# Kernel tuning notes

Hardware: AMD Instinct MI355X
Metric: run time of the kernel (lower is better)

Reference implementation:

```python
import jax, jax.numpy as jnp
import numpy as np

B, T, INPUT_DIM, EMBED_DIM = 64, 512, 512, 256


def _lstm_dir(x, mask, k, r, b):
    """Masked unidirectional LSTM (Keras semantics: masked steps carry prev h/c).
    x: [B,T,D], mask: [B,T] bool, k: [D,4U], r: [U,4U], b: [4U]. Returns [B,T,U]."""
    Bx = x.shape[0]
    U = r.shape[0]
    # Precompute input projection once for all timesteps (gate order: i,f,g,o)
    xz = jnp.einsum('btd,dk->btk', x, k) + b          # [B,T,4U]
    xz_t = jnp.swapaxes(xz, 0, 1)                     # [T,B,4U]
    mask_t = jnp.swapaxes(mask, 0, 1)                 # [T,B]
    h0 = jnp.zeros((Bx, U), x.dtype)
    c0 = jnp.zeros((Bx, U), x.dtype)

    def step(carry, inp):
        h, c = carry
        z_x, m = inp
        z = z_x + h @ r                               # [B,4U]
        i, f, g, o = jnp.split(z, 4, axis=-1)
        i = jax.nn.sigmoid(i)
        f = jax.nn.sigmoid(f)
        g = jnp.tanh(g)
        o = jax.nn.sigmoid(o)
        c_new = f * c + i * g
        h_new = o * jnp.tanh(c_new)
        m = m[:, None]
        h2 = jnp.where(m, h_new, h)                   # carry state through masked steps
        c2 = jnp.where(m, c_new, c)
        return (h2, c2), h2

    _, hs = jax.lax.scan(step, (h0, c0), (xz_t, mask_t))
    return jnp.swapaxes(hs, 0, 1)                     # [B,T,U]


def _bilstm_sum(x, mask, kf, rf, bf, kb, rb, bb):
    fwd = _lstm_dir(x, mask, kf, rf, bf)
    # Keras Bidirectional: reverse input and mask, run, reverse output back
    bwd = _lstm_dir(x[:, ::-1], mask[:, ::-1], kb, rb, bb)[:, ::-1]
    return fwd + bwd                                  # merge_mode='sum'


def _lstm_params(key, d_in, units):
    k1, k2, k3 = jax.random.split(key, 3)
    kernel = jax.random.normal(k1, (d_in, 4 * units), jnp.float32) / np.sqrt(d_in)
    rec = jax.random.normal(k2, (units, 4 * units), jnp.float32) / np.sqrt(units)
    bias = jnp.concatenate([
        jnp.zeros((units,), jnp.float32),
        jnp.ones((units,), jnp.float32),              # unit_forget_bias
        jnp.zeros((2 * units,), jnp.float32),
    ])
    return kernel, rec, bias


def setup_inputs() -> dict:
    key = jax.random.key(0)
    ks = jax.random.split(key, 6)
    sequences = jax.random.normal(ks[0], (B, T, INPUT_DIM), jnp.float32)
    sizes = jax.random.randint(ks[1], (B,), 0, T, jnp.int32)
    enc_kf, enc_rf, enc_bf = _lstm_params(ks[2], INPUT_DIM, EMBED_DIM)
    enc_kb, enc_rb, enc_bb = _lstm_params(ks[3], INPUT_DIM, EMBED_DIM)
    dec_kf, dec_rf, dec_bf = _lstm_params(ks[4], EMBED_DIM, INPUT_DIM)
    dec_kb, dec_rb, dec_bb = _lstm_params(ks[5], EMBED_DIM, INPUT_DIM)
    return {
        'sequences': sequences, 'sizes': sizes,
        'enc_kf': enc_kf, 'enc_rf': enc_rf, 'enc_bf': enc_bf,
        'enc_kb': enc_kb, 'enc_rb': enc_rb, 'enc_bb': enc_bb,
        'dec_kf': dec_kf, 'dec_rf': dec_rf, 'dec_bf': dec_bf,
        'dec_kb': dec_kb, 'dec_rb': dec_rb, 'dec_bb': dec_bb,
    }


def reference(sequences, sizes,
              enc_kf, enc_rf, enc_bf, enc_kb, enc_rb, enc_bb,
              dec_kf, dec_rf, dec_bf, dec_kb, dec_rb, dec_bb):
    mask = jnp.arange(sequences.shape[1])[None, :] < sizes[:, None]   # [B,T]
    x = _bilstm_sum(sequences, mask, enc_kf, enc_rf, enc_bf, enc_kb, enc_rb, enc_bb)
    x = _bilstm_sum(x, mask, dec_kf, dec_rf, dec_bf, dec_kb, dec_rb, dec_bb)
    return x
```

## Files before the change

### kernel.cpp

```cpp
#include <hip/hip_runtime.h>
#include <stdint.h>

using short8 = __attribute__((ext_vector_type(8))) short;
using f32x4  = __attribute__((ext_vector_type(4))) float;

#define DEV static __device__ __forceinline__

DEV unsigned short f2bf(float f){
  unsigned u = __builtin_bit_cast(unsigned, f);
  u = (u + 0x7FFFu + ((u >> 16) & 1u)) >> 16;
  return (unsigned short)u;
}
DEV float sigm(float x){
  float e = __builtin_amdgcn_exp2f(-1.4426950408889634f * x);
  return __builtin_amdgcn_rcpf(1.0f + e);
}
DEV float tanh_(float x){
  float e = __builtin_amdgcn_exp2f(2.885390081777927f * x);
  return 1.0f - 2.0f * __builtin_amdgcn_rcpf(e + 1.0f);
}


__global__ void k_f32_to_bf16(const float* __restrict__ in, unsigned short* __restrict__ out, int n){
  int stride = gridDim.x * blockDim.x * 4;
  for (int i = (blockIdx.x * blockDim.x + threadIdx.x) * 4; i < n; i += stride){
    float4 v = *(const float4*)(in + i);
    ushort4 o4;
    o4.x = f2bf(v.x); o4.y = f2bf(v.y); o4.z = f2bf(v.z); o4.w = f2bf(v.w);
    *(ushort4*)(out + i) = o4;
  }
}

__global__ void k_add_bf16(const float* __restrict__ a, const float* __restrict__ b,
                           unsigned short* __restrict__ out, int n){
  int stride = gridDim.x * blockDim.x * 4;
  for (int i = (blockIdx.x * blockDim.x + threadIdx.x) * 4; i < n; i += stride){
    float4 va = *(const float4*)(a + i);
    float4 vb = *(const float4*)(b + i);
    ushort4 o4;
    o4.x = f2bf(va.x + vb.x); o4.y = f2bf(va.y + vb.y);
    o4.z = f2bf(va.z + vb.z); o4.w = f2bf(va.w + vb.w);
    *(ushort4*)(out + i) = o4;
  }
}

__global__ void k_add_f32(float* __restrict__ o, const float* __restrict__ b, int n){
  int stride = gridDim.x * blockDim.x * 4;
  for (int i = (blockIdx.x * blockDim.x + threadIdx.x) * 4; i < n; i += stride){
    float4 vo = *(const float4*)(o + i);
    float4 vb = *(const float4*)(b + i);
    vo.x += vb.x; vo.y += vb.y; vo.z += vb.z; vo.w += vb.w;
    *(float4*)(o + i) = vo;
  }
}

__global__ void k_pack(const float* __restrict__ k0, const float* __restrict__ r0,
                       const float* __restrict__ k1, const float* __restrict__ r1,
                       unsigned short* __restrict__ out, int E, int KX, int U){
  int n = 2 * E;
  int stride = gridDim.x * blockDim.x;
  for (int i = blockIdx.x * blockDim.x + threadIdx.x; i < n; i += stride){
    int d = i / E, r = i % E;
    const float* Km = d ? k1 : k0;
    const float* Rm = d ? r1 : r0;
    int j    = r & 7;  int q = r >> 3;
    int lane = q & 63; q >>= 6;
    int nt   = q & 3;  q >>= 2;
    int kt   = q % 6;  q /= 6;
    int w    = q & 3;  int wg = q >> 2;
    int k    = (w*6 + kt)*32 + ((lane >> 4) << 3) + j;
    int col  = nt * U + wg*16 + (lane & 15);
    float v  = (k < KX) ? Km[(size_t)k * (4*U) + col]
                        : Rm[(size_t)(k - KX) * (4*U) + col];
    out[i] = f2bf(v);
  }
}

template<int KX, int U, int WGS>
__global__ __launch_bounds__(256, 1)
void lstm_rec(const unsigned short* __restrict__ xab,
              const unsigned short* __restrict__ packedB,
              const float* __restrict__ bias_f,
              const float* __restrict__ bias_b,
              const int*   __restrict__ sizes,
              unsigned short* __restrict__ hbuf,
              unsigned int*  __restrict__ counters,
              float* __restrict__ out_f,
              float* __restrict__ out_b)
{
  constexpr int KTW = 6;
  constexpr int T   = 512;

  const int tid  = threadIdx.x;
  const int w    = tid >> 6;
  const int lane = tid & 63;
  const int dir  = (blockIdx.x >= WGS) ? 1 : 0;
  const int wg   = dir ? (int)blockIdx.x - WGS : (int)blockIdx.x;

  const unsigned short* pB = packedB + (size_t)dir * ((size_t)WGS*4*KTW*4*512)
                                     + (size_t)((wg*4 + w)*KTW)*4*512;
  unsigned short* hb  = hbuf + (size_t)dir * (2*64*U);
  unsigned int*   cnt = counters + dir * 32;
  const float* bias = dir ? bias_b : bias_f;
  float* outp       = dir ? out_b : out_f;

  const bool has_h = ((w*KTW + KTW - 1) * 32) >= KX;

  short8 bfr[KTW][4];
  #pragma unroll
  for (int kt = 0; kt < KTW; ++kt)
    #pragma unroll
    for (int nt = 0; nt < 4; ++nt)
      bfr[kt][nt] = *(const short8*)(pB + ((kt*4 + nt)*512) + lane*8);

  const int u_l = tid & 15;
  const int rb  = (tid >> 4) * 4;
  const int ug  = wg*16 + u_l;
  float bz[4]; int sz[4];
  #pragma unroll
  for (int g = 0; g < 4; ++g) bz[g] = bias[g*U + ug];
  #pragma unroll
  for (int r = 0; r < 4; ++r) sz[r] = sizes[rb + r];
  float c[4]    = {0.f,0.f,0.f,0.f};
  float hreg[4] = {0.f,0.f,0.f,0.f};

  __shared__ float part[4][64][68];

  const int arow  = lane & 15;
  const int kgrp  = (lane >> 4) * 8;
  const int rquad = (lane >> 4) * 4;

  short8 areg[KTW][4];
  {
    const int t0 = dir ? T - 1 : 0;
    #pragma unroll
    for (int kt = 0; kt < KTW; ++kt){
      const int kg = (w*KTW + kt) * 32;
      if (kg < KX){
        #pragma unroll
        for (int mt = 0; mt < 4; ++mt)
          areg[kt][mt] = *(const short8*)(xab + ((size_t)((mt*16 + arow)*T + t0))*KX + (kg + kgrp));
      }
    }
  }

  for (int s = 0; s < T; ++s){
    const int t   = dir ? (T - 1 - s) : s;
    const int par = s & 1;

    f32x4 acc[4][4];
    #pragma unroll
    for (int mt = 0; mt < 4; ++mt)
      #pragma unroll
      for (int nt = 0; nt < 4; ++nt)
        acc[mt][nt] = (f32x4){0.f, 0.f, 0.f, 0.f};

    #pragma unroll
    for (int kt = 0; kt < KTW; ++kt){
      const int kg = (w*KTW + kt) * 32;
      if (kg < KX){
        #pragma unroll
        for (int mt = 0; mt < 4; ++mt)
          #pragma unroll
          for (int nt = 0; nt < 4; ++nt)
            acc[mt][nt] = __builtin_amdgcn_mfma_f32_16x16x32_bf16(areg[kt][mt], bfr[kt][nt], acc[mt][nt], 0, 0, 0);
      }
    }

    if (s > 0){
      if (has_h){
        const unsigned tgt = (unsigned)WGS * (unsigned)s;
        for (;;){
          unsigned v = __hip_atomic_load(cnt, __ATOMIC_RELAXED, __HIP_MEMORY_SCOPE_AGENT);
          if (v >= tgt) break;
          __builtin_amdgcn_s_sleep(1);
        }
        __builtin_amdgcn_sched_barrier(0);
        #pragma unroll
        for (int kt = 0; kt < KTW; ++kt){
          const int kg = (w*KTW + kt) * 32;
          if (kg >= KX){
            #pragma unroll
            for (int mt = 0; mt < 4; ++mt){
              const unsigned long long* hp = (const unsigned long long*)
                  (hb + (size_t)par*64*U + (size_t)(mt*16 + arow)*U + (kg - KX + kgrp));
              ulonglong2 u;
              u.x = __hip_atomic_load(hp,     __ATOMIC_RELAXED, __HIP_MEMORY_SCOPE_AGENT);
              u.y = __hip_atomic_load(hp + 1, __ATOMIC_RELAXED, __HIP_MEMORY_SCOPE_AGENT);
              areg[kt][mt] = __builtin_bit_cast(short8, u);
            }
          }
        }
        #pragma unroll
        for (int kt = 0; kt < KTW; ++kt){
          const int kg = (w*KTW + kt) * 32;
          if (kg >= KX){
            #pragma unroll
            for (int mt = 0; mt < 4; ++mt)
              #pragma unroll
              for (int nt = 0; nt < 4; ++nt)
                acc[mt][nt] = __builtin_amdgcn_mfma_f32_16x16x32_bf16(areg[kt][mt], bfr[kt][nt], acc[mt][nt], 0, 0, 0);
          }
        }
      }
    }

    #pragma unroll
    for (int mt = 0; mt < 4; ++mt)
      #pragma unroll
      for (int nt = 0; nt < 4; ++nt)
        *(f32x4*)&part[w][nt*16 + arow][mt*16 + rquad] = acc[mt][nt];

    __syncthreads();

    f32x4 zg[4];
    #pragma unroll
    for (int g = 0; g < 4; ++g){
      const int cb = g*16 + u_l;
      f32x4 v = *(const f32x4*)&part[0][cb][rb];
      #pragma unroll
      for (int ww = 1; ww < 4; ++ww)
        v += *(const f32x4*)&part[ww][cb][rb];
      zg[g] = v;
    }

    #pragma unroll
    for (int r = 0; r < 4; ++r){
      float ig = sigm (zg[0][r] + bz[0]);
      float fg = sigm (zg[1][r] + bz[1]);
      float gg = tanh_(zg[2][r] + bz[2]);
      float og = sigm (zg[3][r] + bz[3]);
      float cn = fg * c[r] + ig * gg;
      float hn = og * tanh_(cn);
      bool m  = (t < sz[r]);
      c[r] = m ? cn : c[r];
      float h = m ? hn : hreg[r];
      hreg[r] = h;
      __hip_atomic_store(&hb[(size_t)(par ^ 1)*64*U + (size_t)(rb + r)*U + ug],
                         (unsigned short)f2bf(h),
                         __ATOMIC_RELAXED, __HIP_MEMORY_SCOPE_AGENT);
    }

    __syncthreads();

    if (s != T - 1){
      if (tid == 0) atomicAdd(cnt, 1u);
    }

    #pragma unroll
    for (int r = 0; r < 4; ++r)
      outp[((size_t)(rb + r)*T + t)*U + ug] = hreg[r];

    if (s != T - 1){
      const int tn = dir ? t - 1 : t + 1;
      #pragma unroll
      for (int kt = 0; kt < KTW; ++kt){
        const int kg = (w*KTW + kt) * 32;
        if (kg < KX){
          #pragma unroll
          for (int mt = 0; mt < 4; ++mt)
            areg[kt][mt] = *(const short8*)(xab + ((size_t)((mt*16 + arow)*T + tn))*KX + (kg + kgrp));
        }
      }
    }
  }
}


extern "C" void kernel_launch(void* const* d_in, const int* in_sizes, int n_in,
                              void* d_out, int out_size, void* d_ws, size_t ws_size,
                              hipStream_t stream){
  const float* x      = (const float*)d_in[0];
  const int*   sizes  = (const int*)  d_in[1];
  const float* enc_kf = (const float*)d_in[2];
  const float* enc_rf = (const float*)d_in[3];
  const float* enc_bf = (const float*)d_in[4];
  const float* enc_kb = (const float*)d_in[5];
  const float* enc_rb = (const float*)d_in[6];
  const float* enc_bb = (const float*)d_in[7];
  const float* dec_kf = (const float*)d_in[8];
  const float* dec_rf = (const float*)d_in[9];
  const float* dec_bf = (const float*)d_in[10];
  const float* dec_kb = (const float*)d_in[11];
  const float* dec_rb = (const float*)d_in[12];
  const float* dec_bb = (const float*)d_in[13];
  float* out = (float*)d_out;
  char*  ws  = (char*)d_ws;

  const size_t o_xbf   = 0;
  const size_t o_esum  = o_xbf   + 33554432ull;
  const size_t o_pBe   = o_esum  + 16777216ull;
  const size_t o_pBd   = o_pBe   + 3145728ull;
  const size_t o_hfe   = o_pBd   + 6291456ull;
  const size_t o_hbe   = o_hfe   + 33554432ull;
  const size_t o_hbd   = o_hbe   + 33554432ull;
  const size_t o_hbufe = o_hbd   + 67108864ull;
  const size_t o_hbufd = o_hbufe + 131072ull;
  const size_t o_cnte  = o_hbufd + 262144ull;
  const size_t o_cntd  = o_cnte  + 4096ull;
  const size_t total   = o_cntd  + 4096ull;
  if (ws_size < total) return;

  unsigned short* xbf   = (unsigned short*)(ws + o_xbf);
  unsigned short* esum  = (unsigned short*)(ws + o_esum);
  unsigned short* pBe   = (unsigned short*)(ws + o_pBe);
  unsigned short* pBd   = (unsigned short*)(ws + o_pBd);
  float*          hfe   = (float*)(ws + o_hfe);
  float*          hbe   = (float*)(ws + o_hbe);
  float*          hbd   = (float*)(ws + o_hbd);
  unsigned short* hbufe = (unsigned short*)(ws + o_hbufe);
  unsigned short* hbufd = (unsigned short*)(ws + o_hbufd);
  unsigned int*   cnte  = (unsigned int*)(ws + o_cnte);
  unsigned int*   cntd  = (unsigned int*)(ws + o_cntd);

  hipMemsetAsync(ws + o_cnte, 0, 8192ull, stream);

  k_f32_to_bf16<<<2048, 256, 0, stream>>>(x, xbf, 64*512*512);

  k_pack<<<2048, 256, 0, stream>>>(enc_kf, enc_rf, enc_kb, enc_rb, pBe, 786432, 512, 256);
  k_pack<<<2048, 256, 0, stream>>>(dec_kf, dec_rf, dec_kb, dec_rb, pBd, 1572864, 256, 512);

  lstm_rec<512, 256, 16><<<32, 256, 0, stream>>>(xbf, pBe, enc_bf, enc_bb, sizes,
                                                 hbufe, cnte, hfe, hbe);
  k_add_bf16<<<2048, 256, 0, stream>>>(hfe, hbe, esum, 64*512*256);

  lstm_rec<256, 512, 32><<<64, 256, 0, stream>>>(esum, pBd, dec_bf, dec_bb, sizes,
                                                 hbufd, cntd, out, hbd);
  k_add_f32<<<2048, 256, 0, stream>>>(out, hbd, 64*512*512);
}
```

Measured before the change: 5.580 ms.

## Replace global step counter with per-element tagged h exchange between workgroups

New measurement: 10.03 ms. +79.8%, slower.

```diff
diff --git a/kernel.cpp b/kernel.cpp
--- a/kernel.cpp
+++ b/kernel.cpp
@@ -3,6 +3,8 @@
 
 using short8 = __attribute__((ext_vector_type(8))) short;
 using f32x4  = __attribute__((ext_vector_type(4))) float;
+using uint4v = __attribute__((ext_vector_type(4))) unsigned;
+typedef unsigned long long ull;
 
 #define DEV static __device__ __forceinline__
 
@@ -11,6 +13,9 @@
   u = (u + 0x7FFFu + ((u >> 16) & 1u)) >> 16;
   return (unsigned short)u;
 }
+DEV float bf2f(unsigned short v){
+  return __builtin_bit_cast(float, ((unsigned)v) << 16);
+}
 DEV float sigm(float x){
   float e = __builtin_amdgcn_exp2f(-1.4426950408889634f * x);
   return __builtin_amdgcn_rcpf(1.0f + e);
@@ -18,6 +23,32 @@
 DEV float tanh_(float x){
   float e = __builtin_amdgcn_exp2f(2.885390081777927f * x);
   return 1.0f - 2.0f * __builtin_amdgcn_rcpf(e + 1.0f);
+}
+
+DEV void bar_lds(){
+  __builtin_amdgcn_sched_barrier(0);
+  asm volatile("s_waitcnt lgkmcnt(0)" ::: "memory");
+  __builtin_amdgcn_s_barrier();
+  __builtin_amdgcn_sched_barrier(0);
+}
+DEV void bar_plain(){
+  __builtin_amdgcn_sched_barrier(0);
+  __builtin_amdgcn_s_barrier();
+  __builtin_amdgcn_sched_barrier(0);
+}
+
+DEV int frag_ok(const ull d0, const ull d1, const ull d2, const ull d3, ull pat){
+  const ull M = 0xFFFF0000FFFF0000ull;
+  ull v = ((d0 & M) ^ pat) | ((d1 & M) ^ pat) | ((d2 & M) ^ pat) | ((d3 & M) ^ pat);
+  return __all(v == 0);
+}
+DEV short8 unpack_h(const ull d0, const ull d1, const ull d2, const ull d3){
+  uint4v u;
+  u[0] = (unsigned)(d0 & 0xFFFFull) | ((unsigned)(d0 >> 32) << 16);
+  u[1] = (unsigned)(d1 & 0xFFFFull) | ((unsigned)(d1 >> 32) << 16);
+  u[2] = (unsigned)(d2 & 0xFFFFull) | ((unsigned)(d2 >> 32) << 16);
+  u[3] = (unsigned)(d3 & 0xFFFFull) | ((unsigned)(d3 >> 32) << 16);
+  return __builtin_bit_cast(short8, u);
 }
 
 
@@ -31,16 +62,17 @@
   }
 }
 
-__global__ void k_add_bf16(const float* __restrict__ a, const float* __restrict__ b,
-                           unsigned short* __restrict__ out, int n){
-  int stride = gridDim.x * blockDim.x * 4;
-  for (int i = (blockIdx.x * blockDim.x + threadIdx.x) * 4; i < n; i += stride){
-    float4 va = *(const float4*)(a + i);
-    float4 vb = *(const float4*)(b + i);
-    ushort4 o4;
-    o4.x = f2bf(va.x + vb.x); o4.y = f2bf(va.y + vb.y);
-    o4.z = f2bf(va.z + vb.z); o4.w = f2bf(va.w + vb.w);
-    *(ushort4*)(out + i) = o4;
+__global__ void k_add_bb(const unsigned short* __restrict__ a, const unsigned short* __restrict__ b,
+                         unsigned short* __restrict__ out, int n){
+  int stride = gridDim.x * blockDim.x * 8;
+  for (int i = (blockIdx.x * blockDim.x + threadIdx.x) * 8; i < n; i += stride){
+    short8 va = *(const short8*)(a + i);
+    short8 vb = *(const short8*)(b + i);
+    short8 o;
+    #pragma unroll
+    for (int j = 0; j < 8; ++j)
+      o[j] = (short)f2bf(bf2f((unsigned short)va[j]) + bf2f((unsigned short)vb[j]));
+    *(short8*)(out + i) = o;
   }
 }
 
@@ -68,7 +100,7 @@
     int nt   = q & 3;  q >>= 2;
     int kt   = q % 6;  q /= 6;
     int w    = q & 3;  int wg = q >> 2;
-    int k    = (w*6 + kt)*32 + ((lane >> 4) << 3) + j;
+    int k    = (kt*4 + w)*32 + ((lane >> 4) << 3) + j;
     int col  = nt * U + wg*16 + (lane & 15);
     float v  = (k < KX) ? Km[(size_t)k * (4*U) + col]
                         : Rm[(size_t)(k - KX) * (4*U) + col];
@@ -76,19 +108,20 @@
   }
 }
 
-template<int KX, int U, int WGS>
+template<int KX, int U, int WGS, bool OBF>
 __global__ __launch_bounds__(256, 1)
 void lstm_rec(const unsigned short* __restrict__ xab,
               const unsigned short* __restrict__ packedB,
               const float* __restrict__ bias_f,
               const float* __restrict__ bias_b,
               const int*   __restrict__ sizes,
-              unsigned short* __restrict__ hbuf,
-              unsigned int*  __restrict__ counters,
-              float* __restrict__ out_f,
-              float* __restrict__ out_b)
+              unsigned* __restrict__ hbuf2,
+              void* __restrict__ out_f,
+              void* __restrict__ out_b)
 {
   constexpr int KTW = 6;
+  constexpr int XKT = KX / 128;
+  constexpr int NH  = KTW - XKT;
   constexpr int T   = 512;
 
   const int tid  = threadIdx.x;
@@ -99,12 +132,9 @@
 
   const unsigned short* pB = packedB + (size_t)dir * ((size_t)WGS*4*KTW*4*512)
                                      + (size_t)((wg*4 + w)*KTW)*4*512;
-  unsigned short* hb  = hbuf + (size_t)dir * (2*64*U);
-  unsigned int*   cnt = counters + dir * 32;
+  unsigned* hb2     = hbuf2 + (size_t)dir * (2*64*U);
   const float* bias = dir ? bias_b : bias_f;
-  float* outp       = dir ? out_b : out_f;
-
-  const bool has_h = ((w*KTW + KTW - 1) * 32) >= KX;
+  void* outp        = dir ? out_b : out_f;
 
   short8 bfr[KTW][4];
   #pragma unroll
@@ -130,23 +160,40 @@
   const int kgrp  = (lane >> 4) * 8;
   const int rquad = (lane >> 4) * 4;
 
-  short8 areg[KTW][4];
+  short8 xreg[XKT][4];
   {
     const int t0 = dir ? T - 1 : 0;
     #pragma unroll
-    for (int kt = 0; kt < KTW; ++kt){
-      const int kg = (w*KTW + kt) * 32;
-      if (kg < KX){
-        #pragma unroll
-        for (int mt = 0; mt < 4; ++mt)
-          areg[kt][mt] = *(const short8*)(xab + ((size_t)((mt*16 + arow)*T + t0))*KX + (kg + kgrp));
-      }
-    }
-  }
+    for (int kt = 0; kt < XKT; ++kt){
+      const int kg = (kt*4 + w) * 32;
+      #pragma unroll
+      for (int mt = 0; mt < 4; ++mt)
+        xreg[kt][mt] = *(const short8*)(xab + ((size_t)((mt*16 + arow)*T + t0))*KX + (kg + kgrp));
+    }
+  }
+
+  ull raw[NH][4][4];
 
   for (int s = 0; s < T; ++s){
     const int t   = dir ? (T - 1 - s) : s;
     const int par = s & 1;
+    const ull tag = (ull)(unsigned)s;
+    const ull pat = (tag << 16) | (tag << 48);
+    const unsigned* hb2r = hb2 + (size_t)par*64*U;
+
+    if (s > 0){
+      #pragma unroll
+      for (int i = 0; i < NH; ++i){
+        const int hu = ((XKT + i)*4 + w)*32 - KX + kgrp;
+        #pragma unroll
+        for (int mt = 0; mt < 4; ++mt){
+          const ull* hp = (const ull*)(hb2r + (size_t)(mt*16 + arow)*U + hu);
+          #pragma unroll
+          for (int j = 0; j < 4; ++j)
+            raw[i][mt][j] = __hip_atomic_load(hp + j, __ATOMIC_RELAXED, __HIP_MEMORY_SCOPE_AGENT);
+        }
+      }
+    }
 
     f32x4 acc[4][4];
     #pragma unroll
@@ -156,54 +203,55 @@
         acc[mt][nt] = (f32x4){0.f, 0.f, 0.f, 0.f};
 
     #pragma unroll
-    for (int kt = 0; kt < KTW; ++kt){
-      const int kg = (w*KTW + kt) * 32;
-      if (kg < KX){
-        #pragma unroll
-        for (int mt = 0; mt < 4; ++mt)
+    for (int kt = 0; kt < XKT; ++kt)
+      #pragma unroll
+      for (int mt = 0; mt < 4; ++mt)
+        #pragma unroll
+        for (int nt = 0; nt < 4; ++nt)
+          acc[mt][nt] = __builtin_amdgcn_mfma_f32_16x16x32_bf16(xreg[kt][mt], bfr[kt][nt], acc[mt][nt], 0, 0, 0);
+
+    if (s > 0){
+      unsigned bad = (1u << (NH*4)) - 1u;
+      for (;;){
+        unsigned nbad = 0;
+        #pragma unroll
+        for (int i = 0; i < NH; ++i)
           #pragma unroll
-          for (int nt = 0; nt < 4; ++nt)
-            acc[mt][nt] = __builtin_amdgcn_mfma_f32_16x16x32_bf16(areg[kt][mt], bfr[kt][nt], acc[mt][nt], 0, 0, 0);
-      }
-    }
-
-    if (s > 0){
-      if (has_h){
-        const unsigned tgt = (unsigned)WGS * (unsigned)s;
-        for (;;){
-          unsigned v = __hip_atomic_load(cnt, __ATOMIC_RELAXED, __HIP_MEMORY_SCOPE_AGENT);
-          if (v >= tgt) break;
-          __builtin_amdgcn_s_sleep(1);
-        }
-        __builtin_amdgcn_sched_barrier(0);
-        #pragma unroll
-        for (int kt = 0; kt < KTW; ++kt){
-          const int kg = (w*KTW + kt) * 32;
-          if (kg >= KX){
-            #pragma unroll
-            for (int mt = 0; mt < 4; ++mt){
-              const unsigned long long* hp = (const unsigned long long*)
-                  (hb + (size_t)par*64*U + (size_t)(mt*16 + arow)*U + (kg - KX + kgrp));
-              ulonglong2 u;
-              u.x = __hip_atomic_load(hp,     __ATOMIC_RELAXED, __HIP_MEMORY_SCOPE_AGENT);
-              u.y = __hip_atomic_load(hp + 1, __ATOMIC_RELAXED, __HIP_MEMORY_SCOPE_AGENT);
-              areg[kt][mt] = __builtin_bit_cast(short8, u);
+          for (int mt = 0; mt < 4; ++mt){
+            const unsigned f = i*4 + mt;
+            if (bad & (1u << f))
+              if (!frag_ok(raw[i][mt][0], raw[i][mt][1], raw[i][mt][2], raw[i][mt][3], pat))
+                nbad |= 1u << f;
+          }
+        if (!nbad) break;
+        #pragma unroll
+        for (int i = 0; i < NH; ++i){
+          const int hu = ((XKT + i)*4 + w)*32 - KX + kgrp;
+          #pragma unroll
+          for (int mt = 0; mt < 4; ++mt){
+            const unsigned f = i*4 + mt;
+            if (nbad & (1u << f)){
+              const ull* hp = (const ull*)(hb2r + (size_t)(mt*16 + arow)*U + hu);
+              #pragma unroll
+              for (int j = 0; j < 4; ++j)
+                raw[i][mt][j] = __hip_atomic_load(hp + j, __ATOMIC_RELAXED, __HIP_MEMORY_SCOPE_AGENT);
             }
           }
         }
-        #pragma unroll
-        for (int kt = 0; kt < KTW; ++kt){
-          const int kg = (w*KTW + kt) * 32;
-          if (kg >= KX){
-            #pragma unroll
-            for (int mt = 0; mt < 4; ++mt)
-              #pragma unroll
-              for (int nt = 0; nt < 4; ++nt)
-                acc[mt][nt] = __builtin_amdgcn_mfma_f32_16x16x32_bf16(areg[kt][mt], bfr[kt][nt], acc[mt][nt], 0, 0, 0);
-          }
+        bad = nbad;
+      }
+      #pragma unroll
+      for (int i = 0; i < NH; ++i)
+        #pragma unroll
+        for (int mt = 0; mt < 4; ++mt){
+          short8 a = unpack_h(raw[i][mt][0], raw[i][mt][1], raw[i][mt][2], raw[i][mt][3]);
+          #pragma unroll
+          for (int nt = 0; nt < 4; ++nt)
+            acc[mt][nt] = __builtin_amdgcn_mfma_f32_16x16x32_bf16(a, bfr[XKT + i][nt], acc[mt][nt], 0, 0, 0);
         }
-      }
-    }
+    }
+
+    bar_plain();
 
     #pragma unroll
     for (int mt = 0; mt < 4; ++mt)
@@ -211,7 +259,7 @@
       for (int nt = 0; nt < 4; ++nt)
         *(f32x4*)&part[w][nt*16 + arow][mt*16 + rquad] = acc[mt][nt];
 
-    __syncthreads();
+    bar_lds();
 
     f32x4 zg[4];
     #pragma unroll
@@ -224,6 +272,8 @@
       zg[g] = v;
     }
 
+    unsigned* hb2w = hb2 + (size_t)(par ^ 1)*64*U;
+    const unsigned utag = (unsigned)(s + 1) << 16;
     #pragma unroll
     for (int r = 0; r < 4; ++r){
       float ig = sigm (zg[0][r] + bz[0]);
@@ -236,31 +286,23 @@
       c[r] = m ? cn : c[r];
       float h = m ? hn : hreg[r];
       hreg[r] = h;
-      __hip_atomic_store(&hb[(size_t)(par ^ 1)*64*U + (size_t)(rb + r)*U + ug],
-                         (unsigned short)f2bf(h),
-                         __ATOMIC_RELAXED, __HIP_MEMORY_SCOPE_AGENT);
-    }
-
-    __syncthreads();
-
-    if (s != T - 1){
-      if (tid == 0) atomicAdd(cnt, 1u);
-    }
-
-    #pragma unroll
-    for (int r = 0; r < 4; ++r)
-      outp[((size_t)(rb + r)*T + t)*U + ug] = hreg[r];
+      if (s != T - 1)
+        __hip_atomic_store(hb2w + (size_t)(rb + r)*U + ug,
+                           (unsigned)f2bf(h) | utag,
+                           __ATOMIC_RELAXED, __HIP_MEMORY_SCOPE_AGENT);
+      const size_t oi = ((size_t)(rb + r)*T + t)*U + ug;
+      if constexpr (OBF) ((unsigned short*)outp)[oi] = f2bf(h);
+      else               ((float*)outp)[oi] = h;
+    }
 
     if (s != T - 1){
       const int tn = dir ? t - 1 : t + 1;
       #pragma unroll
-      for (int kt = 0; kt < KTW; ++kt){
-        const int kg = (w*KTW + kt) * 32;
-        if (kg < KX){
-          #pragma unroll
-          for (int mt = 0; mt < 4; ++mt)
-            areg[kt][mt] = *(const short8*)(xab + ((size_t)((mt*16 + arow)*T + tn))*KX + (kg + kgrp));
-        }
+      for (int kt = 0; kt < XKT; ++kt){
+        const int kg = (kt*4 + w) * 32;
+        #pragma unroll
+        for (int mt = 0; mt < 4; ++mt)
+          xreg[kt][mt] = *(const short8*)(xab + ((size_t)((mt*16 + arow)*T + tn))*KX + (kg + kgrp));
       }
     }
   }
@@ -287,44 +329,40 @@
   float* out = (float*)d_out;
   char*  ws  = (char*)d_ws;
 
-  const size_t o_xbf   = 0;
-  const size_t o_esum  = o_xbf   + 33554432ull;
-  const size_t o_pBe   = o_esum  + 16777216ull;
-  const size_t o_pBd   = o_pBe   + 3145728ull;
-  const size_t o_hfe   = o_pBd   + 6291456ull;
-  const size_t o_hbe   = o_hfe   + 33554432ull;
-  const size_t o_hbd   = o_hbe   + 33554432ull;
-  const size_t o_hbufe = o_hbd   + 67108864ull;
-  const size_t o_hbufd = o_hbufe + 131072ull;
-  const size_t o_cnte  = o_hbufd + 262144ull;
-  const size_t o_cntd  = o_cnte  + 4096ull;
-  const size_t total   = o_cntd  + 4096ull;
+  const size_t o_xbf  = 0;
+  const size_t o_esum = o_xbf  + 33554432ull;
+  const size_t o_pBe  = o_esum + 16777216ull;
+  const size_t o_pBd  = o_pBe  + 3145728ull;
+  const size_t o_ehf  = o_pBd  + 6291456ull;
+  const size_t o_ehb  = o_ehf  + 16777216ull;
+  const size_t o_dhb  = o_ehb  + 16777216ull;
+  const size_t o_hb2e = o_dhb  + 67108864ull;
+  const size_t o_hb2d = o_hb2e + 262144ull;
+  const size_t total  = o_hb2d + 524288ull;
   if (ws_size < total) return;
 
-  unsigned short* xbf   = (unsigned short*)(ws + o_xbf);
-  unsigned short* esum  = (unsigned short*)(ws + o_esum);
-  unsigned short* pBe   = (unsigned short*)(ws + o_pBe);
-  unsigned short* pBd   = (unsigned short*)(ws + o_pBd);
-  float*          hfe   = (float*)(ws + o_hfe);
-  float*          hbe   = (float*)(ws + o_hbe);
-  float*          hbd   = (float*)(ws + o_hbd);
-  unsigned short* hbufe = (unsigned short*)(ws + o_hbufe);
-  unsigned short* hbufd = (unsigned short*)(ws + o_hbufd);
-  unsigned int*   cnte  = (unsigned int*)(ws + o_cnte);
-  unsigned int*   cntd  = (unsigned int*)(ws + o_cntd);
-
-  hipMemsetAsync(ws + o_cnte, 0, 8192ull, stream);
+  unsigned short* xbf  = (unsigned short*)(ws + o_xbf);
+  unsigned short* esum = (unsigned short*)(ws + o_esum);
+  unsigned short* pBe  = (unsigned short*)(ws + o_pBe);
+  unsigned short* pBd  = (unsigned short*)(ws + o_pBd);
+  unsigned short* ehf  = (unsigned short*)(ws + o_ehf);
+  unsigned short* ehb  = (unsigned short*)(ws + o_ehb);
+  float*          dhb  = (float*)(ws + o_dhb);
+  unsigned*       hb2e = (unsigned*)(ws + o_hb2e);
+  unsigned*       hb2d = (unsigned*)(ws + o_hb2d);
+
+  hipMemsetAsync(ws + o_hb2e, 0, 262144ull + 524288ull, stream);
 
   k_f32_to_bf16<<<2048, 256, 0, stream>>>(x, xbf, 64*512*512);
 
   k_pack<<<2048, 256, 0, stream>>>(enc_kf, enc_rf, enc_kb, enc_rb, pBe, 786432, 512, 256);
   k_pack<<<2048, 256, 0, stream>>>(dec_kf, dec_rf, dec_kb, dec_rb, pBd, 1572864, 256, 512);
 
-  lstm_rec<512, 256, 16><<<32, 256, 0, stream>>>(xbf, pBe, enc_bf, enc_bb, sizes,
-                                                 hbufe, cnte, hfe, hbe);
-  k_add_bf16<<<2048, 256, 0, stream>>>(hfe, hbe, esum, 64*512*256);
-
-  lstm_rec<256, 512, 32><<<64, 256, 0, stream>>>(esum, pBd, dec_bf, dec_bb, sizes,
-                                                 hbufd, cntd, out, hbd);
-  k_add_f32<<<2048, 256, 0, stream>>>(out, hbd, 64*512*512);
-}
+  lstm_rec<512, 256, 16, true><<<32, 256, 0, stream>>>(xbf, pBe, enc_bf, enc_bb, sizes,
+                                                       hb2e, ehf, ehb);
+  k_add_bb<<<2048, 256, 0, stream>>>(ehf, ehb, esum, 64*512*256);
+
+  lstm_rec<256, 512, 32, false><<<64, 256, 0, stream>>>(esum, pBd, dec_bf, dec_bb, sizes,
+                                                        hb2d, out, dhb);
+  k_add_f32<<<2048, 256, 0, stream>>>(out, dhb, 64*512*512);
+}
```

## Replace grid counter with per-wave flags and double-buffer LDS partials

Applied to the files above, without the earlier changes.

New measurement: 6.771 ms. +21.3%, slower.

```diff
diff --git a/kernel.cpp b/kernel.cpp
--- a/kernel.cpp
+++ b/kernel.cpp
@@ -3,6 +3,7 @@
 
 using short8 = __attribute__((ext_vector_type(8))) short;
 using f32x4  = __attribute__((ext_vector_type(4))) float;
+typedef unsigned long long ull;
 
 #define DEV static __device__ __forceinline__
 
@@ -11,6 +12,9 @@
   u = (u + 0x7FFFu + ((u >> 16) & 1u)) >> 16;
   return (unsigned short)u;
 }
+DEV float bf2f(unsigned short v){
+  return __builtin_bit_cast(float, ((unsigned)v) << 16);
+}
 DEV float sigm(float x){
   float e = __builtin_amdgcn_exp2f(-1.4426950408889634f * x);
   return __builtin_amdgcn_rcpf(1.0f + e);
@@ -18,6 +22,13 @@
 DEV float tanh_(float x){
   float e = __builtin_amdgcn_exp2f(2.885390081777927f * x);
   return 1.0f - 2.0f * __builtin_amdgcn_rcpf(e + 1.0f);
+}
+
+DEV void bar_lds(){
+  __builtin_amdgcn_sched_barrier(0);
+  asm volatile("s_waitcnt lgkmcnt(0)" ::: "memory");
+  __builtin_amdgcn_s_barrier();
+  __builtin_amdgcn_sched_barrier(0);
 }
 
 
@@ -31,16 +42,17 @@
   }
 }
 
-__global__ void k_add_bf16(const float* __restrict__ a, const float* __restrict__ b,
-                           unsigned short* __restrict__ out, int n){
-  int stride = gridDim.x * blockDim.x * 4;
-  for (int i = (blockIdx.x * blockDim.x + threadIdx.x) * 4; i < n; i += stride){
-    float4 va = *(const float4*)(a + i);
-    float4 vb = *(const float4*)(b + i);
-    ushort4 o4;
-    o4.x = f2bf(va.x + vb.x); o4.y = f2bf(va.y + vb.y);
-    o4.z = f2bf(va.z + vb.z); o4.w = f2bf(va.w + vb.w);
-    *(ushort4*)(out + i) = o4;
+__global__ void k_add_bb(const unsigned short* __restrict__ a, const unsigned short* __restrict__ b,
+                         unsigned short* __restrict__ out, int n){
+  int stride = gridDim.x * blockDim.x * 8;
+  for (int i = (blockIdx.x * blockDim.x + threadIdx.x) * 8; i < n; i += stride){
+    short8 va = *(const short8*)(a + i);
+    short8 vb = *(const short8*)(b + i);
+    short8 o;
+    #pragma unroll
+    for (int j = 0; j < 8; ++j)
+      o[j] = (short)f2bf(bf2f((unsigned short)va[j]) + bf2f((unsigned short)vb[j]));
+    *(short8*)(out + i) = o;
   }
 }
 
@@ -76,7 +88,7 @@
   }
 }
 
-template<int KX, int U, int WGS>
+template<int KX, int U, int WGS, bool OBF>
 __global__ __launch_bounds__(256, 1)
 void lstm_rec(const unsigned short* __restrict__ xab,
               const unsigned short* __restrict__ packedB,
@@ -84,12 +96,13 @@
               const float* __restrict__ bias_b,
               const int*   __restrict__ sizes,
               unsigned short* __restrict__ hbuf,
-              unsigned int*  __restrict__ counters,
-              float* __restrict__ out_f,
-              float* __restrict__ out_b)
+              unsigned* __restrict__ flags,
+              void* __restrict__ out_f,
+              void* __restrict__ out_b)
 {
   constexpr int KTW = 6;
   constexpr int T   = 512;
+  constexpr int NF  = WGS * 4;
 
   const int tid  = threadIdx.x;
   const int w    = tid >> 6;
@@ -99,10 +112,10 @@
 
   const unsigned short* pB = packedB + (size_t)dir * ((size_t)WGS*4*KTW*4*512)
                                      + (size_t)((wg*4 + w)*KTW)*4*512;
-  unsigned short* hb  = hbuf + (size_t)dir * (2*64*U);
-  unsigned int*   cnt = counters + dir * 32;
-  const float* bias = dir ? bias_b : bias_f;
-  float* outp       = dir ? out_b : out_f;
+  unsigned short* hb = hbuf + (size_t)dir * (2*64*U);
+  unsigned*      flg = flags + (size_t)dir * (NF*32);
+  const float* bias  = dir ? bias_b : bias_f;
+  void* outp         = dir ? out_b : out_f;
 
   const bool has_h = ((w*KTW + KTW - 1) * 32) >= KX;
 
@@ -124,13 +137,13 @@
   float c[4]    = {0.f,0.f,0.f,0.f};
   float hreg[4] = {0.f,0.f,0.f,0.f};
 
-  __shared__ float part[4][64][68];
+  __shared__ float part[2][4][64][68];
 
   const int arow  = lane & 15;
   const int kgrp  = (lane >> 4) * 8;
   const int rquad = (lane >> 4) * 4;
 
-  short8 areg[KTW][4];
+  short8 xreg[KTW][4];
   {
     const int t0 = dir ? T - 1 : 0;
     #pragma unroll
@@ -139,7 +152,7 @@
       if (kg < KX){
         #pragma unroll
         for (int mt = 0; mt < 4; ++mt)
-          areg[kt][mt] = *(const short8*)(xab + ((size_t)((mt*16 + arow)*T + t0))*KX + (kg + kgrp));
+          xreg[kt][mt] = *(const short8*)(xab + ((size_t)((mt*16 + arow)*T + t0))*KX + (kg + kgrp));
       }
     }
   }
@@ -163,44 +176,46 @@
         for (int mt = 0; mt < 4; ++mt)
           #pragma unroll
           for (int nt = 0; nt < 4; ++nt)
-            acc[mt][nt] = __builtin_amdgcn_mfma_f32_16x16x32_bf16(areg[kt][mt], bfr[kt][nt], acc[mt][nt], 0, 0, 0);
-      }
-    }
-
-    if (s > 0){
-      if (has_h){
-        const unsigned tgt = (unsigned)WGS * (unsigned)s;
-        for (;;){
-          unsigned v = __hip_atomic_load(cnt, __ATOMIC_RELAXED, __HIP_MEMORY_SCOPE_AGENT);
-          if (v >= tgt) break;
-          __builtin_amdgcn_s_sleep(1);
+            acc[mt][nt] = __builtin_amdgcn_mfma_f32_16x16x32_bf16(xreg[kt][mt], bfr[kt][nt], acc[mt][nt], 0, 0, 0);
+      }
+    }
+
+    if (s > 0 && has_h){
+      const unsigned tgt = (unsigned)s;
+      for (;;){
+        unsigned v = __hip_atomic_load(&flg[lane*32], __ATOMIC_RELAXED, __HIP_MEMORY_SCOPE_AGENT);
+        if constexpr (NF > 64){
+          unsigned v2 = __hip_atomic_load(&flg[(lane + 64)*32], __ATOMIC_RELAXED, __HIP_MEMORY_SCOPE_AGENT);
+          v = v2 < v ? v2 : v;
         }
-        __builtin_amdgcn_sched_barrier(0);
-        #pragma unroll
-        for (int kt = 0; kt < KTW; ++kt){
-          const int kg = (w*KTW + kt) * 32;
-          if (kg >= KX){
-            #pragma unroll
-            for (int mt = 0; mt < 4; ++mt){
-              const unsigned long long* hp = (const unsigned long long*)
-                  (hb + (size_t)par*64*U + (size_t)(mt*16 + arow)*U + (kg - KX + kgrp));
-              ulonglong2 u;
-              u.x = __hip_atomic_load(hp,     __ATOMIC_RELAXED, __HIP_MEMORY_SCOPE_AGENT);
-              u.y = __hip_atomic_load(hp + 1, __ATOMIC_RELAXED, __HIP_MEMORY_SCOPE_AGENT);
-              areg[kt][mt] = __builtin_bit_cast(short8, u);
-            }
+        if (__all(v >= tgt)) break;
+        __builtin_amdgcn_s_sleep(1);
+      }
+      __builtin_amdgcn_sched_barrier(0);
+      short8 hregs[KTW][4];
+      #pragma unroll
+      for (int kt = 0; kt < KTW; ++kt){
+        const int kg = (w*KTW + kt) * 32;
+        if (kg >= KX){
+          #pragma unroll
+          for (int mt = 0; mt < 4; ++mt){
+            const ull* hp = (const ull*)(hb + (size_t)par*64*U + (size_t)(mt*16 + arow)*U + (kg - KX + kgrp));
+            ulonglong2 u;
+            u.x = __hip_atomic_load(hp,     __ATOMIC_RELAXED, __HIP_MEMORY_SCOPE_AGENT);
+            u.y = __hip_atomic_load(hp + 1, __ATOMIC_RELAXED, __HIP_MEMORY_SCOPE_AGENT);
+            hregs[kt][mt] = __builtin_bit_cast(short8, u);
           }
         }
-        #pragma unroll
-        for (int kt = 0; kt < KTW; ++kt){
-          const int kg = (w*KTW + kt) * 32;
-          if (kg >= KX){
+      }
+      #pragma unroll
+      for (int kt = 0; kt < KTW; ++kt){
+        const int kg = (w*KTW + kt) * 32;
+        if (kg >= KX){
+          #pragma unroll
+          for (int mt = 0; mt < 4; ++mt)
             #pragma unroll
-            for (int mt = 0; mt < 4; ++mt)
-              #pragma unroll
-              for (int nt = 0; nt < 4; ++nt)
-                acc[mt][nt] = __builtin_amdgcn_mfma_f32_16x16x32_bf16(areg[kt][mt], bfr[kt][nt], acc[mt][nt], 0, 0, 0);
-          }
+            for (int nt = 0; nt < 4; ++nt)
+              acc[mt][nt] = __builtin_amdgcn_mfma_f32_16x16x32_bf16(hregs[kt][mt], bfr[kt][nt], acc[mt][nt], 0, 0, 0);
         }
       }
     }
@@ -209,18 +224,18 @@
     for (int mt = 0; mt < 4; ++mt)
       #pragma unroll
       for (int nt = 0; nt < 4; ++nt)
-        *(f32x4*)&part[w][nt*16 + arow][mt*16 + rquad] = acc[mt][nt];
-
-    __syncthreads();
+        *(f32x4*)&part[par][w][nt*16 + arow][mt*16 + rquad] = acc[mt][nt];
+
+    bar_lds();
 
     f32x4 zg[4];
     #pragma unroll
     for (int g = 0; g < 4; ++g){
       const int cb = g*16 + u_l;
-      f32x4 v = *(const f32x4*)&part[0][cb][rb];
+      f32x4 v = *(const f32x4*)&part[par][0][cb][rb];
       #pragma unroll
       for (int ww = 1; ww < 4; ++ww)
-        v += *(const f32x4*)&part[ww][cb][rb];
+        v += *(const f32x4*)&part[par][ww][cb][rb];
       zg[g] = v;
     }
 
@@ -236,20 +251,28 @@
       c[r] = m ? cn : c[r];
       float h = m ? hn : hreg[r];
       hreg[r] = h;
-      __hip_atomic_store(&hb[(size_t)(par ^ 1)*64*U + (size_t)(rb + r)*U + ug],
-                         (unsigned short)f2bf(h),
-                         __ATOMIC_RELAXED, __HIP_MEMORY_SCOPE_AGENT);
-    }
-
-    __syncthreads();
+      if (s != T - 1)
+        __hip_atomic_store(&hb[(size_t)(par ^ 1)*64*U + (size_t)(rb + r)*U + ug],
+                           (unsigned short)f2bf(h),
+                           __ATOMIC_RELAXED, __HIP_MEMORY_SCOPE_AGENT);
+    }
 
     if (s != T - 1){
-      if (tid == 0) atomicAdd(cnt, 1u);
-    }
-
-    #pragma unroll
-    for (int r = 0; r < 4; ++r)
-      outp[((size_t)(rb + r)*T + t)*U + ug] = hreg[r];
+      __builtin_amdgcn_sched_barrier(0);
+      asm volatile("s_waitcnt vmcnt(0)" ::: "memory");
+      __builtin_amdgcn_sched_barrier(0);
+      if (lane == 0)
+        __hip_atomic_store(&flg[(wg*4 + w)*32], (unsigned)(s + 1),
+                           __ATOMIC_RELAXED, __HIP_MEMORY_SCOPE_AGENT);
+      __builtin_amdgcn_sched_barrier(0);
+    }
+
+    #pragma unroll
+    for (int r = 0; r < 4; ++r){
+      const size_t oi = ((size_t)(rb + r)*T + t)*U + ug;
+      if constexpr (OBF) ((unsigned short*)outp)[oi] = f2bf(hreg[r]);
+      else               ((float*)outp)[oi] = hreg[r];
+    }
 
     if (s != T - 1){
       const int tn = dir ? t - 1 : t + 1;
@@ -259,7 +282,7 @@
         if (kg < KX){
           #pragma unroll
           for (int mt = 0; mt < 4; ++mt)
-            areg[kt][mt] = *(const short8*)(xab + ((size_t)((mt*16 + arow)*T + tn))*KX + (kg + kgrp));
+            xreg[kt][mt] = *(const short8*)(xab + ((size_t)((mt*16 + arow)*T + tn))*KX + (kg + kgrp));
         }
       }
     }
@@ -291,40 +314,40 @@
   const size_t o_esum  = o_xbf   + 33554432ull;
   const size_t o_pBe   = o_esum  + 16777216ull;
   const size_t o_pBd   = o_pBe   + 3145728ull;
-  const size_t o_hfe   = o_pBd   + 6291456ull;
-  const size_t o_hbe   = o_hfe   + 33554432ull;
-  const size_t o_hbd   = o_hbe   + 33554432ull;
-  const size_t o_hbufe = o_hbd   + 67108864ull;
+  const size_t o_ehf   = o_pBd   + 6291456ull;
+  const size_t o_ehb   = o_ehf   + 16777216ull;
+  const size_t o_dhb   = o_ehb   + 16777216ull;
+  const size_t o_hbufe = o_dhb   + 67108864ull;
   const size_t o_hbufd = o_hbufe + 131072ull;
-  const size_t o_cnte  = o_hbufd + 262144ull;
-  const size_t o_cntd  = o_cnte  + 4096ull;
-  const size_t total   = o_cntd  + 4096ull;
+  const size_t o_flge  = o_hbufd + 262144ull;
+  const size_t o_flgd  = o_flge  + 16384ull;
+  const size_t total   = o_flgd  + 32768ull;
   if (ws_size < total) return;
 
   unsigned short* xbf   = (unsigned short*)(ws + o_xbf);
   unsigned short* esum  = (unsigned short*)(ws + o_esum);
   unsigned short* pBe   = (unsigned short*)(ws + o_pBe);
   unsigned short* pBd   = (unsigned short*)(ws + o_pBd);
-  float*          hfe   = (float*)(ws + o_hfe);
-  float*          hbe   = (float*)(ws + o_hbe);
-  float*          hbd   = (float*)(ws + o_hbd);
+  unsigned short* ehf   = (unsigned short*)(ws + o_ehf);
+  unsigned short* ehb   = (unsigned short*)(ws + o_ehb);
+  float*          dhb   = (float*)(ws + o_dhb);
   unsigned short* hbufe = (unsigned short*)(ws + o_hbufe);
   unsigned short* hbufd = (unsigned short*)(ws + o_hbufd);
-  unsigned int*   cnte  = (unsigned int*)(ws + o_cnte);
-  unsigned int*   cntd  = (unsigned int*)(ws + o_cntd);
-
-  hipMemsetAsync(ws + o_cnte, 0, 8192ull, stream);
+  unsigned*       flge  = (unsigned*)(ws + o_flge);
+  unsigned*       flgd  = (unsigned*)(ws + o_flgd);
+
+  hipMemsetAsync(ws + o_flge, 0, 16384ull + 32768ull, stream);
 
   k_f32_to_bf16<<<2048, 256, 0, stream>>>(x, xbf, 64*512*512);
 
   k_pack<<<2048, 256, 0, stream>>>(enc_kf, enc_rf, enc_kb, enc_rb, pBe, 786432, 512, 256);
   k_pack<<<2048, 256, 0, stream>>>(dec_kf, dec_rf, dec_kb, dec_rb, pBd, 1572864, 256, 512);
 
-  lstm_rec<512, 256, 16><<<32, 256, 0, stream>>>(xbf, pBe, enc_bf, enc_bb, sizes,
-                                                 hbufe, cnte, hfe, hbe);
-  k_add_bf16<<<2048, 256, 0, stream>>>(hfe, hbe, esum, 64*512*256);
-
-  lstm_rec<256, 512, 32><<<64, 256, 0, stream>>>(esum, pBd, dec_bf, dec_bb, sizes,
-                                                 hbufd, cntd, out, hbd);
-  k_add_f32<<<2048, 256, 0, stream>>>(out, hbd, 64*512*512);
-}
+  lstm_rec<512, 256, 16, true><<<32, 256, 0, stream>>>(xbf, pBe, enc_bf, enc_bb, sizes,
+                                                       hbufe, flge, ehf, ehb);
+  k_add_bb<<<2048, 256, 0, stream>>>(ehf, ehb, esum, 64*512*256);
+
+  lstm_rec<256, 512, 32, false><<<64, 256, 0, stream>>>(esum, pBd, dec_bf, dec_bb, sizes,
+                                                        hbufd, flgd, out, dhb);
+  k_add_f32<<<2048, 256, 0, stream>>>(out, dhb, 64*512*512);
+}
```
